# Kernel tuning notes

Measured on AMD Instinct MI355X. Metric: run time of the kernel, lower is better.

## Reference

```python
import jax, jax.numpy as jnp
import numpy as np

N, F, C, E = 1024, 64, 4, 32768
H = 256       # MLP hidden width
C_OUT = 4     # new edge channels produced by nn_edge


def setup_inputs() -> dict:
    key = jax.random.key(0)
    ks = jax.random.split(key, 12)
    x = jax.random.normal(ks[0], (N, F), dtype=jnp.float32)
    edge_index = jax.random.randint(ks[1], (C, 2, E), 0, N)
    edge_weight = jax.random.uniform(ks[2], (C, E), dtype=jnp.float32)
    s_n1 = 1.0 / np.sqrt(C * F)
    s_n2 = 1.0 / np.sqrt(H)
    s_e1 = 1.0 / np.sqrt(C + 2 * F)
    return {
        "x": x,
        "edge_index": edge_index,
        "edge_weight": edge_weight,
        "Wn1": jax.random.normal(ks[3], (C * F, H), dtype=jnp.float32) * s_n1,
        "bn1": jnp.zeros((H,), jnp.float32),
        "Wn2": jax.random.normal(ks[4], (H, F), dtype=jnp.float32) * s_n2,
        "bn2": jnp.zeros((F,), jnp.float32),
        "We1": jax.random.normal(ks[5], (C + 2 * F, H), dtype=jnp.float32) * s_e1,
        "be1": jnp.zeros((H,), jnp.float32),
        "We2": jax.random.normal(ks[6], (H, C_OUT), dtype=jnp.float32) * s_n2,
        "be2": jnp.zeros((C_OUT,), jnp.float32),
        "eps": jnp.zeros((), jnp.float32),
    }


def reference(x, edge_index, edge_weight, Wn1, bn1, Wn2, bn2, We1, be1, We2, be2, eps):
    # ---- MCGNN: per-channel edge-weighted scatter-add aggregation ----
    def agg_one(ei, w):
        # ei: [2,E] (row0 = source j, row1 = target i); w: [E]
        msg = x[ei[0]] * w[:, None]                       # [E,F]
        return jax.ops.segment_sum(msg, ei[1], num_segments=N)  # [N,F]

    agg = jax.vmap(agg_one)(edge_index, edge_weight)      # [C,N,F]
    out_cat = agg + (1.0 + eps) * x                       # broadcast self term
    h = out_cat.transpose(1, 0, 2).reshape(N, C * F)      # [N, C*F]
    x_next = jax.nn.relu(h @ Wn1 + bn1) @ Wn2 + bn2       # [N,F]

    # ---- EDPGNN: dense adjacency per channel + broadcast x_i/x_j ----
    def dense_adj(ei, w):
        return jnp.zeros((N, N), x.dtype).at[ei[0], ei[1]].add(w)

    a = jax.vmap(dense_adj)(edge_index, edge_weight)      # [C,N,N]
    a = a.transpose(1, 2, 0)                              # [N,N,C]
    x_i = jnp.broadcast_to(x_next[:, None, :], (N, N, F))
    x_j = jnp.broadcast_to(x_next[None, :, :], (N, N, F))
    feat = jnp.concatenate([a, x_i, x_j], axis=2).reshape(N * N, C + 2 * F)
    adj_out = (jax.nn.relu(feat @ We1 + be1) @ We2 + be2).reshape(N, N, C_OUT)
    return adj_out
```

## Files before the change

kernel.cpp:

```cpp
#include <hip/hip_runtime.h>

#define NN 1024
#define FF 64
#define CC 4
#define EE 32768
#define HH 256

#define OFF_ADENSE 0u
#define OFF_CNT    4194304u
#define OFF_MASK   4198400u
#define OFF_OFFS   4231168u
#define OFF_CURSOR 4235268u
#define OFF_SRTS   4239364u
#define OFF_SRTW   4370436u
#define OFF_P      4501508u
#define OFF_Q      4763652u

__global__ __launch_bounds__(256)
void k_count(const int* __restrict__ ei, int* __restrict__ cnt)
{
    unsigned t = blockIdx.x * 256u + threadIdx.x;
    unsigned e = t & (EE - 1u);
    unsigned c = t >> 15;
    int dst = ei[c * 2 * EE + EE + e];
    atomicAdd(&cnt[c * NN + dst], 1);
}

__global__ __launch_bounds__(256)
void k_scan(const int* __restrict__ cnt, int* __restrict__ offs, int* __restrict__ cursor)
{
    __shared__ int wsum[4];
    const int t = threadIdx.x;
    int c[16];
    int s = 0;
    const int4* cp = (const int4*)(cnt + t * 16);
#pragma unroll
    for (int u = 0; u < 4; ++u) {
        int4 v = cp[u];
        c[u * 4 + 0] = v.x; c[u * 4 + 1] = v.y; c[u * 4 + 2] = v.z; c[u * 4 + 3] = v.w;
        s += v.x + v.y + v.z + v.w;
    }
    int incl = s;
#pragma unroll
    for (int d = 1; d < 64; d <<= 1) {
        int v = __shfl_up(incl, d, 64);
        if ((t & 63) >= d) incl += v;
    }
    const int w = t >> 6;
    if ((t & 63) == 63) wsum[w] = incl;
    __syncthreads();
    int base = incl - s;
    for (int ww = 0; ww < w; ++ww) base += wsum[ww];
    int run = base;
#pragma unroll
    for (int u = 0; u < 16; ++u) {
        offs[t * 16 + u] = run;
        cursor[t * 16 + u] = run;
        run += c[u];
    }
    if (t == 255) offs[4096] = run;
}

__global__ __launch_bounds__(256)
void k_bucket_adj(const int* __restrict__ ei, const float* __restrict__ ew,
                  int* __restrict__ cursor, int* __restrict__ srt_src,
                  float* __restrict__ srt_w, float* __restrict__ adense,
                  unsigned* __restrict__ mask)
{
    unsigned t = blockIdx.x * 256u + threadIdx.x;
    unsigned e = t & (EE - 1u);
    unsigned c = t >> 15;
    int src = ei[c * 2 * EE + e];
    int dst = ei[c * 2 * EE + EE + e];
    float w = ew[c * EE + e];
    int pos = atomicAdd(&cursor[c * NN + dst], 1);
    srt_src[pos] = src;
    srt_w[pos] = w;
    unsigned pair = (unsigned)src * NN + (unsigned)dst;
    atomicAdd(&adense[(size_t)pair * CC + c], w);
    atomicOr(&mask[pair >> 5], 1u << (pair & 31u));
}

__global__ __launch_bounds__(1024)
void k_node(const float* __restrict__ x, const int* __restrict__ offs,
            const int* __restrict__ srt_src, const float* __restrict__ srt_w,
            const float* __restrict__ Wn1, const float* __restrict__ bn1,
            const float* __restrict__ Wn2, const float* __restrict__ bn2,
            const float* __restrict__ We1, const float* __restrict__ be1,
            const float* __restrict__ epsp,
            float* __restrict__ P, float* __restrict__ Q)
{
    __shared__ float hval[4][256];
    __shared__ float hidl[4][256];
    __shared__ float part[4][4][64];
    __shared__ float xnl[4][64];
    const int tid = threadIdx.x;
    const int n0 = blockIdx.x * 4;

    {
        const int w = tid >> 6, lane = tid & 63;
        const int c = w & 3, nn = w >> 2;
        const int g = c * NN + (n0 + nn);
        const int beg = offs[g], end = offs[g + 1];
        float acc = 0.f;
        for (int k = beg; k < end; ++k)
            acc += x[srt_src[k] * FF + lane] * srt_w[k];
        const float ope = 1.0f + epsp[0];
        hval[nn][c * 64 + lane] = acc + ope * x[(n0 + nn) * FF + lane];
    }
    __syncthreads();

    {
        const int nn = tid >> 8, h = tid & 255;
        float acc = bn1[h];
#pragma unroll 8
        for (int k = 0; k < 256; ++k)
            acc += hval[nn][k] * Wn1[k * 256 + h];
        hidl[nn][h] = fmaxf(acc, 0.f);
    }
    __syncthreads();

    {
        const int kq = tid >> 8, nn = (tid >> 6) & 3, f = tid & 63;
        float p = 0.f;
#pragma unroll 8
        for (int k = kq * 64; k < kq * 64 + 64; ++k)
            p += hidl[nn][k] * Wn2[k * 64 + f];
        part[kq][nn][f] = p;
    }
    __syncthreads();
    if (tid < 256) {
        const int nn = tid >> 6, f = tid & 63;
        xnl[nn][f] = bn2[f] + part[0][nn][f] + part[1][nn][f]
                             + part[2][nn][f] + part[3][nn][f];
    }
    __syncthreads();

    {
        const int r = tid >> 8, h = tid & 255;
        float p = be1[h], q = 0.f;
#pragma unroll 8
        for (int f = 0; f < 64; ++f) {
            float xv = xnl[r][f];
            p += xv * We1[(4 + f) * 256 + h];
            q += xv * We1[(68 + f) * 256 + h];
        }
        P[(n0 + r) * 256 + h] = p;
        Q[(n0 + r) * 256 + h] = q;
    }
}

__global__ __launch_bounds__(256, 4)
void k_edge_mlp(const float* __restrict__ P, const float* __restrict__ Q,
                const float* __restrict__ adense, const unsigned* __restrict__ mask,
                const float* __restrict__ We1,
                const float* __restrict__ We2, const float* __restrict__ be2,
                float* __restrict__ out)
{
    __shared__ float4 SMEM[1024];
    __shared__ int nzlist[1024];
    __shared__ int lcnt;

    const int tid = threadIdx.x;
    const int tx = tid & 15, ty = tid >> 4;
    const int iBase = blockIdx.y * 32, jBase = blockIdx.x * 32;
    const int psw = ty & 7;
    const int qsw = tx & 7;

    if (tid == 0) lcnt = 0;
    __syncthreads();

    unsigned nzmask = 0;
    float4 acc[2][2];
    {
        const unsigned m0 = mask[(unsigned)(iBase + ty * 2 + 0) * 32u + ((unsigned)jBase >> 5)];
        const unsigned m1 = mask[(unsigned)(iBase + ty * 2 + 1) * 32u + ((unsigned)jBase >> 5)];
#pragma unroll
        for (int ii = 0; ii < 2; ++ii)
#pragma unroll
            for (int jj = 0; jj < 2; ++jj) {
                const unsigned m = ii ? m1 : m0;
                if ((m >> (tx * 2 + jj)) & 1u) {
                    nzmask |= 1u << (ii * 2 + jj);
                    int idx = atomicAdd(&lcnt, 1);
                    nzlist[idx] = (ty * 2 + ii) * 32 + (tx * 2 + jj);
                }
                acc[ii][jj] = make_float4(0.f, 0.f, 0.f, 0.f);
            }
    }

    for (int hc = 0; hc < 4; ++hc) {
        __syncthreads();
#pragma unroll
        for (int u = 0; u < 2; ++u) {
            int idx = tid + u * 256;
            int row = idx >> 4, q = idx & 15;
            int ph = q ^ ((row >> 1) & 7);
            SMEM[row * 16 + ph]       = *(const float4*)(P + (iBase + row) * 256 + hc * 64 + q * 4);
            SMEM[512 + row * 16 + ph] = *(const float4*)(Q + (jBase + row) * 256 + hc * 64 + q * 4);
        }
        __syncthreads();

        for (int q = 0; q < 16; ++q) {
            float4 w2[4];
#pragma unroll
            for (int k = 0; k < 4; ++k)
                w2[k] = *(const float4*)(We2 + (hc * 64 + q * 4 + k) * 4);

            float4 p[2], qv[2];
#pragma unroll
            for (int r = 0; r < 2; ++r) p[r]  = SMEM[(ty * 2 + r) * 16 + (q ^ psw)];
#pragma unroll
            for (int r = 0; r < 2; ++r) qv[r] = SMEM[512 + (tx * 2 + r) * 16 + (q ^ qsw)];

#pragma unroll
            for (int ii = 0; ii < 2; ++ii) {
#pragma unroll
                for (int jj = 0; jj < 2; ++jj) {
                    float v0 = fmaxf(p[ii].x + qv[jj].x, 0.f);
                    float v1 = fmaxf(p[ii].y + qv[jj].y, 0.f);
                    float v2 = fmaxf(p[ii].z + qv[jj].z, 0.f);
                    float v3 = fmaxf(p[ii].w + qv[jj].w, 0.f);
                    acc[ii][jj].x += v0 * w2[0].x + v1 * w2[1].x + v2 * w2[2].x + v3 * w2[3].x;
                    acc[ii][jj].y += v0 * w2[0].y + v1 * w2[1].y + v2 * w2[2].y + v3 * w2[3].y;
                    acc[ii][jj].z += v0 * w2[0].z + v1 * w2[1].z + v2 * w2[2].z + v3 * w2[3].z;
                    acc[ii][jj].w += v0 * w2[0].w + v1 * w2[1].w + v2 * w2[2].w + v3 * w2[3].w;
                }
            }
        }
    }

    __syncthreads();
    {
        const int wv = tid >> 6, lane = tid & 63;
        const int nfix = lcnt;
        for (int pi = wv; pi < nfix; pi += 4) {
            const int lij = nzlist[pi];
            const int gi = iBase + (lij >> 5), gj = jBase + (lij & 31);
            const float4 a = *(const float4*)(adense + ((size_t)gi * NN + gj) * 4);
            float o0 = 0.f, o1 = 0.f, o2 = 0.f, o3 = 0.f;
#pragma unroll
            for (int u = 0; u < 4; ++u) {
                const int h = u * 64 + lane;
                float s = a.x * We1[0 * 256 + h] + a.y * We1[1 * 256 + h]
                        + a.z * We1[2 * 256 + h] + a.w * We1[3 * 256 + h];
                float v = fmaxf(P[gi * 256 + h] + Q[gj * 256 + h] + s, 0.f);
                const float4 w2 = *(const float4*)(We2 + h * 4);
                o0 += v * w2.x; o1 += v * w2.y; o2 += v * w2.z; o3 += v * w2.w;
            }
#pragma unroll
            for (int d = 32; d > 0; d >>= 1) {
                o0 += __shfl_down(o0, d, 64);
                o1 += __shfl_down(o1, d, 64);
                o2 += __shfl_down(o2, d, 64);
                o3 += __shfl_down(o3, d, 64);
            }
            if (lane == 0)
                SMEM[lij] = make_float4(o0, o1, o2, o3);
        }
    }
    __syncthreads();

    const float4 b2 = *(const float4*)be2;
#pragma unroll
    for (int ii = 0; ii < 2; ++ii)
#pragma unroll
        for (int jj = 0; jj < 2; ++jj) {
            const int lij = (ty * 2 + ii) * 32 + (tx * 2 + jj);
            const float4 fx = SMEM[lij];
            float4 o = (nzmask & (1u << (ii * 2 + jj))) ? fx : acc[ii][jj];
            o.x += b2.x; o.y += b2.y; o.z += b2.z; o.w += b2.w;
            *(float4*)(out + ((size_t)(iBase + ty * 2 + ii) * NN + (jBase + tx * 2 + jj)) * 4) = o;
        }
}

extern "C" void kernel_launch(void* const* d_in, const int* in_sizes, int n_in,
                              void* d_out, int out_size, void* d_ws, size_t ws_size,
                              hipStream_t stream)
{
    (void)in_sizes; (void)n_in; (void)out_size; (void)ws_size;
    const float* x   = (const float*)d_in[0];
    const int*   ei  = (const int*)d_in[1];
    const float* ew  = (const float*)d_in[2];
    const float* Wn1 = (const float*)d_in[3];
    const float* bn1 = (const float*)d_in[4];
    const float* Wn2 = (const float*)d_in[5];
    const float* bn2 = (const float*)d_in[6];
    const float* We1 = (const float*)d_in[7];
    const float* be1 = (const float*)d_in[8];
    const float* We2 = (const float*)d_in[9];
    const float* be2 = (const float*)d_in[10];
    const float* eps = (const float*)d_in[11];
    float* out = (float*)d_out;

    float*    ws     = (float*)d_ws;
    float*    adense = ws + OFF_ADENSE;
    int*      cnt    = (int*)(ws + OFF_CNT);
    unsigned* mask   = (unsigned*)(ws + OFF_MASK);
    int*      offs   = (int*)(ws + OFF_OFFS);
    int*      cursor = (int*)(ws + OFF_CURSOR);
    int*      srts   = (int*)(ws + OFF_SRTS);
    float*    srtw   = ws + OFF_SRTW;
    float*    Pb     = ws + OFF_P;
    float*    Qb     = ws + OFF_Q;

    (void)hipMemsetAsync(d_ws, 0, (size_t)4231168 * sizeof(float), stream);

    k_count     <<<(CC * EE) / 256, 256, 0, stream>>>(ei, cnt);
    k_scan      <<<1, 256, 0, stream>>>(cnt, offs, cursor);
    k_bucket_adj<<<(CC * EE) / 256, 256, 0, stream>>>(ei, ew, cursor, srts, srtw,
                                                      adense, mask);
    k_node      <<<NN / 4, 1024, 0, stream>>>(x, offs, srts, srtw,
                                              Wn1, bn1, Wn2, bn2, We1, be1, eps, Pb, Qb);

    dim3 g(NN / 32, NN / 32);
    k_edge_mlp<<<g, 256, 0, stream>>>(Pb, Qb, adense, mask, We1, We2, be2, out);
}
```

Measured before the change: 231.0 us.

## Fuse dense adjacency zeroing into count kernel and software-pipeline edge MLP loads

The 16 MB dense adjacency buffer is no longer cleared with a large memset. Instead the count kernel zeroes it with float4 stores, each of 512 blocks clearing 2048 float4s, and the memset only covers the count and mask regions. The edge-MLP inner loop now prefetches the next iteration's We2 and shared-memory P/Q values before computing the current one, to hide load latency. This raises register pressure. Correctness depends on the count kernel finishing before the bucket kernel writes into adense, which stream order guarantees.

Result: no change. 229.7 us (-0.6%).

```diff
diff --git a/kernel.cpp b/kernel.cpp
--- a/kernel.cpp
+++ b/kernel.cpp
@@ -17,13 +17,20 @@
 #define OFF_Q      4763652u
 
 __global__ __launch_bounds__(256)
-void k_count(const int* __restrict__ ei, int* __restrict__ cnt)
+void k_count(const int* __restrict__ ei, int* __restrict__ cnt,
+             float4* __restrict__ adense4)
 {
     unsigned t = blockIdx.x * 256u + threadIdx.x;
     unsigned e = t & (EE - 1u);
     unsigned c = t >> 15;
     int dst = ei[c * 2 * EE + EE + e];
     atomicAdd(&cnt[c * NN + dst], 1);
+
+    const unsigned base = blockIdx.x * 2048u + threadIdx.x;
+    const float4 z = make_float4(0.f, 0.f, 0.f, 0.f);
+#pragma unroll
+    for (int u = 0; u < 8; ++u)
+        adense4[base + u * 256u] = z;
 }
 
 __global__ __launch_bounds__(256)
@@ -201,32 +208,45 @@
         }
         __syncthreads();
 
+        float4 w2c[4], pc[2], qc[2];
+#pragma unroll
+        for (int k = 0; k < 4; ++k)
+            w2c[k] = *(const float4*)(We2 + (hc * 64 + 0 * 4 + k) * 4);
+#pragma unroll
+        for (int r = 0; r < 2; ++r) pc[r] = SMEM[(ty * 2 + r) * 16 + (0 ^ psw)];
+#pragma unroll
+        for (int r = 0; r < 2; ++r) qc[r] = SMEM[512 + (tx * 2 + r) * 16 + (0 ^ qsw)];
+
         for (int q = 0; q < 16; ++q) {
-            float4 w2[4];
+            const int qn = (q + 1) & 15;
+            float4 w2n[4], pn[2], qn_[2];
 #pragma unroll
             for (int k = 0; k < 4; ++k)
-                w2[k] = *(const float4*)(We2 + (hc * 64 + q * 4 + k) * 4);
-
-            float4 p[2], qv[2];
-#pragma unroll
-            for (int r = 0; r < 2; ++r) p[r]  = SMEM[(ty * 2 + r) * 16 + (q ^ psw)];
-#pragma unroll
-            for (int r = 0; r < 2; ++r) qv[r] = SMEM[512 + (tx * 2 + r) * 16 + (q ^ qsw)];
+                w2n[k] = *(const float4*)(We2 + (hc * 64 + qn * 4 + k) * 4);
+#pragma unroll
+            for (int r = 0; r < 2; ++r) pn[r]  = SMEM[(ty * 2 + r) * 16 + (qn ^ psw)];
+#pragma unroll
+            for (int r = 0; r < 2; ++r) qn_[r] = SMEM[512 + (tx * 2 + r) * 16 + (qn ^ qsw)];
 
 #pragma unroll
             for (int ii = 0; ii < 2; ++ii) {
 #pragma unroll
                 for (int jj = 0; jj < 2; ++jj) {
-                    float v0 = fmaxf(p[ii].x + qv[jj].x, 0.f);
-                    float v1 = fmaxf(p[ii].y + qv[jj].y, 0.f);
-                    float v2 = fmaxf(p[ii].z + qv[jj].z, 0.f);
-                    float v3 = fmaxf(p[ii].w + qv[jj].w, 0.f);
-                    acc[ii][jj].x += v0 * w2[0].x + v1 * w2[1].x + v2 * w2[2].x + v3 * w2[3].x;
-                    acc[ii][jj].y += v0 * w2[0].y + v1 * w2[1].y + v2 * w2[2].y + v3 * w2[3].y;
-                    acc[ii][jj].z += v0 * w2[0].z + v1 * w2[1].z + v2 * w2[2].z + v3 * w2[3].z;
-                    acc[ii][jj].w += v0 * w2[0].w + v1 * w2[1].w + v2 * w2[2].w + v3 * w2[3].w;
+                    float v0 = fmaxf(pc[ii].x + qc[jj].x, 0.f);
+                    float v1 = fmaxf(pc[ii].y + qc[jj].y, 0.f);
+                    float v2 = fmaxf(pc[ii].z + qc[jj].z, 0.f);
+                    float v3 = fmaxf(pc[ii].w + qc[jj].w, 0.f);
+                    acc[ii][jj].x += v0 * w2c[0].x + v1 * w2c[1].x + v2 * w2c[2].x + v3 * w2c[3].x;
+                    acc[ii][jj].y += v0 * w2c[0].y + v1 * w2c[1].y + v2 * w2c[2].y + v3 * w2c[3].y;
+                    acc[ii][jj].z += v0 * w2c[0].z + v1 * w2c[1].z + v2 * w2c[2].z + v3 * w2c[3].z;
+                    acc[ii][jj].w += v0 * w2c[0].w + v1 * w2c[1].w + v2 * w2c[2].w + v3 * w2c[3].w;
                 }
             }
+
+#pragma unroll
+            for (int k = 0; k < 4; ++k) w2c[k] = w2n[k];
+#pragma unroll
+            for (int r = 0; r < 2; ++r) { pc[r] = pn[r]; qc[r] = qn_[r]; }
         }
     }
 
@@ -304,9 +324,9 @@
     float*    Pb     = ws + OFF_P;
     float*    Qb     = ws + OFF_Q;
 
-    (void)hipMemsetAsync(d_ws, 0, (size_t)4231168 * sizeof(float), stream);
-
-    k_count     <<<(CC * EE) / 256, 256, 0, stream>>>(ei, cnt);
+    (void)hipMemsetAsync((void*)cnt, 0, (size_t)(4096 + 32768) * sizeof(int), stream);
+
+    k_count     <<<(CC * EE) / 256, 256, 0, stream>>>(ei, cnt, (float4*)adense);
     k_scan      <<<1, 256, 0, stream>>>(cnt, offs, cursor);
     k_bucket_adj<<<(CC * EE) / 256, 256, 0, stream>>>(ei, ew, cursor, srts, srtw,
                                                       adense, mask);
```

## Restructure edge MLP to one pair per thread with transposed Q layout

Applied to the files above, without the earlier changes.

Adds a kernel that transposes Q into an h-quad-major layout so each lane reads coalesced Q values for its own j. The edge MLP now gives each thread one (i,j) pair, with P broadcast per wave via readfirstlane, and drops the shared-memory tiling. Occupancy rises to 8 blocks per SM. The adjacency zeroing moves from a large memset into k_count, which reduces memset traffic. The cost is that per-thread work no longer reuses P/Q through registers and relies on cache for the P and We2 loads.

New measurement: 231.6 us. Within noise of the previous version (+0.3%).

```diff
diff --git a/kernel.cpp b/kernel.cpp
--- a/kernel.cpp
+++ b/kernel.cpp
@@ -15,15 +15,23 @@
 #define OFF_SRTW   4370436u
 #define OFF_P      4501508u
 #define OFF_Q      4763652u
+#define OFF_QT     5025796u
 
 __global__ __launch_bounds__(256)
-void k_count(const int* __restrict__ ei, int* __restrict__ cnt)
+void k_count(const int* __restrict__ ei, int* __restrict__ cnt,
+             float4* __restrict__ adense4)
 {
     unsigned t = blockIdx.x * 256u + threadIdx.x;
     unsigned e = t & (EE - 1u);
     unsigned c = t >> 15;
     int dst = ei[c * 2 * EE + EE + e];
     atomicAdd(&cnt[c * NN + dst], 1);
+
+    const unsigned base = blockIdx.x * 2048u + threadIdx.x;
+    const float4 z = make_float4(0.f, 0.f, 0.f, 0.f);
+#pragma unroll
+    for (int u = 0; u < 8; ++u)
+        adense4[base + u * 256u] = z;
 }
 
 __global__ __launch_bounds__(256)
@@ -150,93 +158,77 @@
     }
 }
 
-__global__ __launch_bounds__(256, 4)
+__global__ __launch_bounds__(256)
+void k_qt(const float4* __restrict__ Q4, float4* __restrict__ QTP)
+{
+    __shared__ float4 qt[32 * 64];
+    const int t = threadIdx.x;
+    const int n0 = blockIdx.x * 32;
+#pragma unroll
+    for (int u = 0; u < 8; ++u) {
+        int idx = t + u * 256;
+        int row = idx >> 6, quad = idx & 63;
+        qt[row * 64 + (quad ^ (row & 7))] = Q4[(n0 + row) * 64 + quad];
+    }
+    __syncthreads();
+#pragma unroll
+    for (int u = 0; u < 8; ++u) {
+        int idx = t + u * 256;
+        int hq = idx >> 5, jl = idx & 31;
+        QTP[hq * NN + n0 + jl] = qt[jl * 64 + (hq ^ (jl & 7))];
+    }
+}
+
+__global__ __launch_bounds__(256, 8)
 void k_edge_mlp(const float* __restrict__ P, const float* __restrict__ Q,
-                const float* __restrict__ adense, const unsigned* __restrict__ mask,
-                const float* __restrict__ We1,
+                const float4* __restrict__ QTP, const float* __restrict__ adense,
+                const unsigned* __restrict__ mask, const float* __restrict__ We1,
                 const float* __restrict__ We2, const float* __restrict__ be2,
                 float* __restrict__ out)
 {
-    __shared__ float4 SMEM[1024];
-    __shared__ int nzlist[1024];
+    __shared__ float4 delta[256];
+    __shared__ int nzlist[256];
     __shared__ int lcnt;
 
     const int tid = threadIdx.x;
-    const int tx = tid & 15, ty = tid >> 4;
-    const int iBase = blockIdx.y * 32, jBase = blockIdx.x * 32;
-    const int psw = ty & 7;
-    const int qsw = tx & 7;
+    const int w = tid >> 6, lane = tid & 63;
+    const int iBase = blockIdx.y * 4, jBase = blockIdx.x * 64;
+    const int i = __builtin_amdgcn_readfirstlane(iBase + w);
+    const int j = jBase + lane;
 
     if (tid == 0) lcnt = 0;
     __syncthreads();
 
-    unsigned nzmask = 0;
-    float4 acc[2][2];
-    {
-        const unsigned m0 = mask[(unsigned)(iBase + ty * 2 + 0) * 32u + ((unsigned)jBase >> 5)];
-        const unsigned m1 = mask[(unsigned)(iBase + ty * 2 + 1) * 32u + ((unsigned)jBase >> 5)];
-#pragma unroll
-        for (int ii = 0; ii < 2; ++ii)
-#pragma unroll
-            for (int jj = 0; jj < 2; ++jj) {
-                const unsigned m = ii ? m1 : m0;
-                if ((m >> (tx * 2 + jj)) & 1u) {
-                    nzmask |= 1u << (ii * 2 + jj);
-                    int idx = atomicAdd(&lcnt, 1);
-                    nzlist[idx] = (ty * 2 + ii) * 32 + (tx * 2 + jj);
-                }
-                acc[ii][jj] = make_float4(0.f, 0.f, 0.f, 0.f);
-            }
-    }
-
-    for (int hc = 0; hc < 4; ++hc) {
-        __syncthreads();
-#pragma unroll
-        for (int u = 0; u < 2; ++u) {
-            int idx = tid + u * 256;
-            int row = idx >> 4, q = idx & 15;
-            int ph = q ^ ((row >> 1) & 7);
-            SMEM[row * 16 + ph]       = *(const float4*)(P + (iBase + row) * 256 + hc * 64 + q * 4);
-            SMEM[512 + row * 16 + ph] = *(const float4*)(Q + (jBase + row) * 256 + hc * 64 + q * 4);
-        }
-        __syncthreads();
-
-        for (int q = 0; q < 16; ++q) {
-            float4 w2[4];
-#pragma unroll
-            for (int k = 0; k < 4; ++k)
-                w2[k] = *(const float4*)(We2 + (hc * 64 + q * 4 + k) * 4);
-
-            float4 p[2], qv[2];
-#pragma unroll
-            for (int r = 0; r < 2; ++r) p[r]  = SMEM[(ty * 2 + r) * 16 + (q ^ psw)];
-#pragma unroll
-            for (int r = 0; r < 2; ++r) qv[r] = SMEM[512 + (tx * 2 + r) * 16 + (q ^ qsw)];
-
-#pragma unroll
-            for (int ii = 0; ii < 2; ++ii) {
-#pragma unroll
-                for (int jj = 0; jj < 2; ++jj) {
-                    float v0 = fmaxf(p[ii].x + qv[jj].x, 0.f);
-                    float v1 = fmaxf(p[ii].y + qv[jj].y, 0.f);
-                    float v2 = fmaxf(p[ii].z + qv[jj].z, 0.f);
-                    float v3 = fmaxf(p[ii].w + qv[jj].w, 0.f);
-                    acc[ii][jj].x += v0 * w2[0].x + v1 * w2[1].x + v2 * w2[2].x + v3 * w2[3].x;
-                    acc[ii][jj].y += v0 * w2[0].y + v1 * w2[1].y + v2 * w2[2].y + v3 * w2[3].y;
-                    acc[ii][jj].z += v0 * w2[0].z + v1 * w2[1].z + v2 * w2[2].z + v3 * w2[3].z;
-                    acc[ii][jj].w += v0 * w2[0].w + v1 * w2[1].w + v2 * w2[2].w + v3 * w2[3].w;
-                }
-            }
-        }
-    }
-
-    __syncthreads();
-    {
-        const int wv = tid >> 6, lane = tid & 63;
+    const unsigned mw = mask[(unsigned)i * 32u + ((unsigned)j >> 5)];
+    const bool nz = (mw >> (j & 31)) & 1u;
+    if (nz) { int idx = atomicAdd(&lcnt, 1); nzlist[idx] = tid; }
+
+    const float4* P4  = (const float4*)P;
+    const float4* W24 = (const float4*)We2;
+    float ax = 0.f, ay = 0.f, az = 0.f, aw = 0.f;
+    for (int hq = 0; hq < 64; ++hq) {
+        const float4 qv  = QTP[hq * NN + j];
+        const float4 pv  = P4[(size_t)i * 64 + hq];
+        const float4 w20 = W24[hq * 4 + 0];
+        const float4 w21 = W24[hq * 4 + 1];
+        const float4 w22 = W24[hq * 4 + 2];
+        const float4 w23 = W24[hq * 4 + 3];
+        const float v0 = fmaxf(pv.x + qv.x, 0.f);
+        const float v1 = fmaxf(pv.y + qv.y, 0.f);
+        const float v2 = fmaxf(pv.z + qv.z, 0.f);
+        const float v3 = fmaxf(pv.w + qv.w, 0.f);
+        ax += v0 * w20.x + v1 * w21.x + v2 * w22.x + v3 * w23.x;
+        ay += v0 * w20.y + v1 * w21.y + v2 * w22.y + v3 * w23.y;
+        az += v0 * w20.z + v1 * w21.z + v2 * w22.z + v3 * w23.z;
+        aw += v0 * w20.w + v1 * w21.w + v2 * w22.w + v3 * w23.w;
+    }
+
+    __syncthreads();
+    {
         const int nfix = lcnt;
-        for (int pi = wv; pi < nfix; pi += 4) {
+        for (int pi = w; pi < nfix; pi += 4) {
             const int lij = nzlist[pi];
-            const int gi = iBase + (lij >> 5), gj = jBase + (lij & 31);
+            const int gi = iBase + (lij >> 6), gj = jBase + (lij & 63);
             const float4 a = *(const float4*)(adense + ((size_t)gi * NN + gj) * 4);
             float o0 = 0.f, o1 = 0.f, o2 = 0.f, o3 = 0.f;
 #pragma unroll
@@ -245,7 +237,7 @@
                 float s = a.x * We1[0 * 256 + h] + a.y * We1[1 * 256 + h]
                         + a.z * We1[2 * 256 + h] + a.w * We1[3 * 256 + h];
                 float v = fmaxf(P[gi * 256 + h] + Q[gj * 256 + h] + s, 0.f);
-                const float4 w2 = *(const float4*)(We2 + h * 4);
+                const float4 w2 = W24[h];
                 o0 += v * w2.x; o1 += v * w2.y; o2 += v * w2.z; o3 += v * w2.w;
             }
 #pragma unroll
@@ -256,22 +248,19 @@
                 o3 += __shfl_down(o3, d, 64);
             }
             if (lane == 0)
-                SMEM[lij] = make_float4(o0, o1, o2, o3);
+                delta[lij] = make_float4(o0, o1, o2, o3);
         }
     }
     __syncthreads();
 
     const float4 b2 = *(const float4*)be2;
-#pragma unroll
-    for (int ii = 0; ii < 2; ++ii)
-#pragma unroll
-        for (int jj = 0; jj < 2; ++jj) {
-            const int lij = (ty * 2 + ii) * 32 + (tx * 2 + jj);
-            const float4 fx = SMEM[lij];
-            float4 o = (nzmask & (1u << (ii * 2 + jj))) ? fx : acc[ii][jj];
-            o.x += b2.x; o.y += b2.y; o.z += b2.z; o.w += b2.w;
-            *(float4*)(out + ((size_t)(iBase + ty * 2 + ii) * NN + (jBase + tx * 2 + jj)) * 4) = o;
-        }
+    const float4 dfx = delta[tid];
+    float4 o;
+    o.x = (nz ? dfx.x : ax) + b2.x;
+    o.y = (nz ? dfx.y : ay) + b2.y;
+    o.z = (nz ? dfx.z : az) + b2.z;
+    o.w = (nz ? dfx.w : aw) + b2.w;
+    *(float4*)(out + ((size_t)i * NN + j) * 4) = o;
 }
 
 extern "C" void kernel_launch(void* const* d_in, const int* in_sizes, int n_in,
@@ -303,16 +292,19 @@
     float*    srtw   = ws + OFF_SRTW;
     float*    Pb     = ws + OFF_P;
     float*    Qb     = ws + OFF_Q;
-
-    (void)hipMemsetAsync(d_ws, 0, (size_t)4231168 * sizeof(float), stream);
-
-    k_count     <<<(CC * EE) / 256, 256, 0, stream>>>(ei, cnt);
+    float*    QTb    = ws + OFF_QT;
+
+    (void)hipMemsetAsync((void*)cnt, 0, (size_t)(4096 + 32768) * sizeof(int), stream);
+
+    k_count     <<<(CC * EE) / 256, 256, 0, stream>>>(ei, cnt, (float4*)adense);
     k_scan      <<<1, 256, 0, stream>>>(cnt, offs, cursor);
     k_bucket_adj<<<(CC * EE) / 256, 256, 0, stream>>>(ei, ew, cursor, srts, srtw,
                                                       adense, mask);
     k_node      <<<NN / 4, 1024, 0, stream>>>(x, offs, srts, srtw,
                                               Wn1, bn1, Wn2, bn2, We1, be1, eps, Pb, Qb);
-
-    dim3 g(NN / 32, NN / 32);
-    k_edge_mlp<<<g, 256, 0, stream>>>(Pb, Qb, adense, mask, We1, We2, be2, out);
-}
+    k_qt        <<<NN / 32, 256, 0, stream>>>((const float4*)Qb, (float4*)QTb);
+
+    dim3 g(NN / 64, NN / 4);
+    k_edge_mlp<<<g, 256, 0, stream>>>(Pb, Qb, (const float4*)QTb, adense, mask,
+                                      We1, We2, be2, out);
+}
```
